# Kernel tuning notes

Hardware: AMD Instinct MI355X
Metric: run time of the kernel (lower is better)

## Reference

```python
import jax, jax.numpy as jnp
import numpy as np

N = 262144            # number of particles
H0 = 0.006            # base SPH support radius (unit square domain)
GRID = 256            # static upper bound on cells per dimension (actual ~170)
NUM_CELLS = GRID * GRID
K = 32                # max particles stored per cell (avg occupancy ~9.4)
NCAND = 9 * K         # searchRadius=1 -> 3x3 cell stencil
MAX_NEIGHBORS = 64    # padded neighbor-list width (avg neighbor count ~27)


def setup_inputs() -> dict:
    key = jax.random.key(0)
    kp, ks = jax.random.split(key)
    positions = jax.random.uniform(kp, (N, 2), dtype=jnp.float32)
    # supports in [0.9*H0, H0], mimicking mildly adaptive SPH supports
    supports = H0 * (0.9 + 0.1 * jax.random.uniform(ks, (N,), dtype=jnp.float32))
    return {"positions": positions, "supports": supports}


def _cell_linear_indices(positions, supports):
    # mirrors sortPositions: cell size = hMax, indices = ceil((p - qMin)/hMax)
    hMax = jnp.max(supports)
    qMin = jnp.min(positions, axis=0) - hMax
    ij = jnp.ceil((positions - qMin) / hMax).astype(jnp.int32)  # >= 1 by construction
    ij = jnp.clip(ij, 0, GRID - 1)
    return ij[:, 0] + GRID * ij[:, 1]


def _build_cell_table(lin):
    # dense equivalent of the hash-grid: sort by cell, counting-sort into [cell, slot]
    order = jnp.argsort(lin)                       # == sortingIndices in the original
    lin_s = lin[order]
    counts = jax.ops.segment_sum(jnp.ones(N, jnp.int32), lin, num_segments=NUM_CELLS)
    starts = jnp.cumsum(counts) - counts           # exclusive prefix sum == cumCell
    rank = jnp.arange(N, dtype=jnp.int32) - starts[lin_s].astype(jnp.int32)
    ovf = rank >= K                                # overflow slots -> dump row
    cell_t = jnp.where(ovf, NUM_CELLS, lin_s)
    slot_t = jnp.where(ovf, 0, rank)
    table = jnp.full((NUM_CELLS + 1, K), -1, dtype=jnp.int32)
    table = table.at[cell_t, slot_t].set(order.astype(jnp.int32))
    return table


def reference(positions, supports):
    lin = _cell_linear_indices(positions, supports)
    table = _build_cell_table(lin)

    # 3x3 stencil of neighbor cells (searchRadius = 1)
    dx, dy = jnp.meshgrid(jnp.arange(-1, 2), jnp.arange(-1, 2), indexing='ij')
    offs = (dx + GRID * dy).reshape(1, 9).astype(jnp.int32)
    cand_cells = jnp.clip(lin[:, None] + offs, 0, NUM_CELLS)  # [N, 9]

    cand = table[cand_cells].reshape(N, NCAND)     # [N, 288] candidate particle ids
    present = cand >= 0
    cidx = jnp.where(present, cand, 0)
    cpos = positions[cidx]                         # [N, 288, 2] gather (memory bound)
    diff = cpos - positions[:, None, :]
    dist = jnp.sqrt(jnp.sum(diff * diff, axis=-1)) # [N, 288]
    valid = present & (dist <= supports[:, None])  # |x_i - x_j| <= h_i (self included)
    count = jnp.sum(valid, axis=1).astype(jnp.int32)

    # compact valid candidates to the front, pad to MAX_NEIGHBORS
    order2 = jnp.argsort(jnp.where(valid, 0, 1).astype(jnp.int32), axis=1, stable=True)
    sel = order2[:, :MAX_NEIGHBORS]
    nbr = jnp.take_along_axis(cidx, sel, axis=1)
    dsel = jnp.take_along_axis(dist, sel, axis=1)
    inb = jnp.arange(MAX_NEIGHBORS)[None, :] < count[:, None]
    neighbors = jnp.where(inb, nbr, -1)
    radial = jnp.where(inb, dsel / supports[:, None], 0.0)  # fluidRadialDistances
    return neighbors, count, radial
```

## Files before the change

kernel.cpp:

```cpp
#include <hip/hip_runtime.h>
#include <float.h>

#define N_PART 262144
#define GRID_DIM 256
#define NUM_CELLS (GRID_DIM * GRID_DIM)
#define KP 32
#define MAXNB 64


__global__ __launch_bounds__(256) void prep_kernel(
        const float2* __restrict__ pos2, const float* __restrict__ sup,
        int* __restrict__ counts,
        float* __restrict__ bMinX, float* __restrict__ bMinY,
        float* __restrict__ bMaxH) {
    __shared__ unsigned s_minx, s_miny, s_maxh;
    int t = threadIdx.x, b = blockIdx.x;
    int tid = b * 256 + t;
    if (tid <= NUM_CELLS) counts[tid] = 0;
    if (t == 0) { s_minx = 0x7f7fffffu; s_miny = 0x7f7fffffu; s_maxh = 0u; }
    __syncthreads();
    float2 p = pos2[tid];
    float  h = sup[tid];
    atomicMin(&s_minx, __float_as_uint(p.x));
    atomicMin(&s_miny, __float_as_uint(p.y));
    atomicMax(&s_maxh, __float_as_uint(h));
    __syncthreads();
    if (t == 0) {
        bMinX[b] = __uint_as_float(s_minx);
        bMinY[b] = __uint_as_float(s_miny);
        bMaxH[b] = __uint_as_float(s_maxh);
    }
}

__global__ __launch_bounds__(256) void bin_kernel(
        const float2* __restrict__ pos2, const float* __restrict__ sup,
        const float* __restrict__ bMinX, const float* __restrict__ bMinY,
        const float* __restrict__ bMaxH,
        unsigned* __restrict__ params,
        int* __restrict__ counts, float4* __restrict__ Qraw) {
    __shared__ unsigned s_minx, s_miny, s_maxh;
    int t = threadIdx.x;
    int tid = blockIdx.x * 256 + t;
    if (t == 0) { s_minx = 0x7f7fffffu; s_miny = 0x7f7fffffu; s_maxh = 0u; }
    __syncthreads();
    {
        float mx = FLT_MAX, my = FLT_MAX, mh = 0.0f;
        for (int k = t; k < 1024; k += 256) {
            mx = fminf(mx, bMinX[k]);
            my = fminf(my, bMinY[k]);
            mh = fmaxf(mh, bMaxH[k]);
        }
        atomicMin(&s_minx, __float_as_uint(mx));
        atomicMin(&s_miny, __float_as_uint(my));
        atomicMax(&s_maxh, __float_as_uint(mh));
    }
    __syncthreads();
    if (blockIdx.x == 0 && t == 0) {
        params[0] = s_minx; params[1] = s_miny; params[2] = s_maxh;
    }
    float hmax  = __uint_as_float(s_maxh);
    float qminx = __uint_as_float(s_minx) - hmax;
    float qminy = __uint_as_float(s_miny) - hmax;
    float2 p = pos2[tid];
    float  h = sup[tid];
    int cx = (int)ceilf((p.x - qminx) / hmax);
    int cy = (int)ceilf((p.y - qminy) / hmax);
    cx = min(max(cx, 0), GRID_DIM - 1);
    cy = min(max(cy, 0), GRID_DIM - 1);
    int c = cx + GRID_DIM * cy;
    int slot = atomicAdd(&counts[c], 1);
    if (slot < KP)
        Qraw[(c << 5) + slot] = make_float4(p.x, p.y, __int_as_float(tid), h);
}

__global__ __launch_bounds__(256) void rank_kernel(
        const int* __restrict__ counts, const float4* __restrict__ Qraw,
        float4* __restrict__ Qpad, int* __restrict__ linR,
        int4* __restrict__ cinfo) {
    int tid = blockIdx.x * 256 + threadIdx.x;
    int c   = tid >> 3;
    int s0  = tid & 7;
    int cnt = min(counts[c], KP);
    const float4* row = Qraw + (c << 5);
    for (int sl = s0; sl < cnt; sl += 8) {
        float4 rec = row[sl];
        int id = __float_as_int(rec.z);
        int rank = 0;
        for (int k = 0; k < cnt; k++)
            rank += (__float_as_int(row[k].z) < id);
        float h = rec.w;
        float  hn  = __int_as_float(__float_as_int(h) + 1);
        double mid = 0.5 * ((double)h + (double)hn);
        double t2  = mid * mid;
        float  S   = (float)t2;
        S = ((double)S > t2) ? __int_as_float(__float_as_int(S) - 1) : S;
        Qpad[(c << 5) + rank] = make_float4(rec.x, rec.y, rec.z, S);
        linR[id] = (c << 5) | rank;
    }
    if (s0 == 0) {
        const int offs[9] = {-257, -1, 255, -256, 0, 256, -255, 1, 257};
        int cum = 0;
        int v[9];
#pragma unroll
        for (int o = 0; o < 9; o++) {
            int cl = min(max(c + offs[o], 0), NUM_CELLS);
            cum += min(counts[cl], KP);
            v[o] = cum;
        }
        cinfo[(c << 2) + 0] = make_int4(v[0], v[1], v[2], v[3]);
        cinfo[(c << 2) + 1] = make_int4(v[4], v[5], v[6], v[7]);
        cinfo[(c << 2) + 2] = make_int4(v[8], 0, 0, 0);
    }
}

__global__ __launch_bounds__(256) void query_kernel(
        const int* __restrict__ linR, const int4* __restrict__ cinfo,
        const float4* __restrict__ Qpad,
        float* __restrict__ outN, float* __restrict__ outC,
        float* __restrict__ outR) {
#pragma clang fp contract(off)
    __shared__ int   s_id[4][MAXNB];
    __shared__ float s_s2[4][MAXNB];

    int t    = threadIdx.x;
    int lane = t & 63;
    int wsl  = t >> 6;
    int bid  = blockIdx.x;
    int swz  = (bid & 7) * (int)(gridDim.x >> 3) + (bid >> 3);
    int w    = __builtin_amdgcn_readfirstlane(swz * 4 + wsl);

    int lr = __builtin_amdgcn_readfirstlane(linR[w]);
    int c  = lr >> 5;

    int4 ca = cinfo[(c << 2) + 0];
    int4 cb = cinfo[(c << 2) + 1];
    int4 cz = cinfo[(c << 2) + 2];
    float4 me = Qpad[lr];
    float px = me.x, py = me.y, S = me.w;

    const int offs[9] = {-257, -1, 255, -256, 0, 256, -255, 1, 257};
    int cum[10] = {0, ca.x, ca.y, ca.z, ca.w, cb.x, cb.y, cb.z, cb.w, };
    cum[9] = cz.x;
    int T = cum[9];
    int delta[9];
#pragma unroll
    for (int o = 0; o < 9; o++) {
        int cl = min(max(c + offs[o], 0), NUM_CELLS);
        delta[o] = (cl << 5) - cum[o];
    }

    if (T <= 64) {
        int dsel = delta[0];
#pragma unroll
        for (int m = 1; m < 9; m++)
            dsel = (lane >= cum[m]) ? delta[m] : dsel;
        int idx = (lane < T) ? (lane + dsel) : lr;
        float4 q = Qpad[idx];
        unsigned long long maskT = (T >= 64) ? ~0ull : ((1ull << T) - 1ull);
        float dx = q.x - px;
        float dy = q.y - py;
        float s2 = dx * dx + dy * dy;
        bool keep = (s2 <= S) && (lane < T);
        unsigned long long bal = __ballot(s2 <= S) & maskT;
        int rank = __builtin_amdgcn_mbcnt_hi(
            (unsigned)(bal >> 32),
            __builtin_amdgcn_mbcnt_lo((unsigned)bal, 0));
        if (keep) {
            s_id[wsl][rank] = __float_as_int(q.z);
            s_s2[wsl][rank] = s2;
        }
        int total = (int)__popcll(bal);
        int   jj = s_id[wsl][lane];
        float ss = s_s2[wsl][lane];
        bool inb = lane < total;
        float rh = __builtin_amdgcn_rsqf(S);
        float vN = inb ? (float)jj : -1.0f;
        float vR = inb ? __builtin_amdgcn_sqrtf(ss) * rh : 0.0f;
        size_t base = (size_t)w * MAXNB;
        __builtin_nontemporal_store(vN, &outN[base + lane]);
        __builtin_nontemporal_store(vR, &outR[base + lane]);
        if (lane == 0)
            __builtin_nontemporal_store((float)total, &outC[w]);
    } else {
        int total = 0;
        for (int b0 = 0; b0 < T; b0 += 64) {
            int ll = b0 + lane;
            int dsel = delta[0];
#pragma unroll
            for (int m = 1; m < 9; m++)
                dsel = (ll >= cum[m]) ? delta[m] : dsel;
            float4 q = Qpad[ll + dsel];
            float dx = q.x - px;
            float dy = q.y - py;
            float s2 = dx * dx + dy * dy;
            int rem = T - b0;
            unsigned long long maskT =
                (rem >= 64) ? ~0ull : ((1ull << rem) - 1ull);
            unsigned long long bal = __ballot(s2 <= S) & maskT;
            int rank = __builtin_amdgcn_mbcnt_hi(
                (unsigned)(bal >> 32),
                __builtin_amdgcn_mbcnt_lo((unsigned)bal, 0));
            int ww = total + rank;
            if ((s2 <= S) && (ll < T) && (ww < MAXNB)) {
                s_id[wsl][ww] = __float_as_int(q.z);
                s_s2[wsl][ww] = s2;
            }
            total += (int)__popcll(bal);
        }
        int stored = min(total, MAXNB);
        int   jj = s_id[wsl][lane];
        float ss = s_s2[wsl][lane];
        bool inb = lane < stored;
        float rh = __builtin_amdgcn_rsqf(S);
        float vN = inb ? (float)jj : -1.0f;
        float vR = inb ? __builtin_amdgcn_sqrtf(ss) * rh : 0.0f;
        size_t base = (size_t)w * MAXNB;
        __builtin_nontemporal_store(vN, &outN[base + lane]);
        __builtin_nontemporal_store(vR, &outR[base + lane]);
        if (lane == 0)
            __builtin_nontemporal_store((float)total, &outC[w]);
    }
}

extern "C" void kernel_launch(void* const* d_in, const int* in_sizes, int n_in,
                              void* d_out, int out_size, void* d_ws, size_t ws_size,
                              hipStream_t stream) {
    const float2* pos2 = (const float2*)d_in[0];
    const float*  sup  = (const float*)d_in[1];

    char* p = (char*)d_ws;
    auto alloc = [&](size_t bytes) {
        char* q = p;
        p += (bytes + 255) & ~(size_t)255;
        return q;
    };
    unsigned* params = (unsigned*)alloc(256);
    int*    counts = (int*)alloc((size_t)(NUM_CELLS + 1) * 4);
    float*  bMinX  = (float*)alloc(1024 * 4);
    float*  bMinY  = (float*)alloc(1024 * 4);
    float*  bMaxH  = (float*)alloc(1024 * 4);
    float4* Qraw   = (float4*)alloc((size_t)(NUM_CELLS + 1) * KP * 16);
    float4* Qpad   = (float4*)alloc(((size_t)(NUM_CELLS + 1) * KP + 64) * 16);
    int*    linR   = (int*)alloc((size_t)N_PART * 4);
    int4*   cinfo  = (int4*)alloc((size_t)NUM_CELLS * 4 * 16);

    float* out  = (float*)d_out;
    float* outN = out;
    float* outC = out + (size_t)N_PART * MAXNB;
    float* outR = outC + N_PART;

    prep_kernel<<<N_PART / 256, 256, 0, stream>>>(pos2, sup, counts,
                                                  bMinX, bMinY, bMaxH);
    bin_kernel<<<N_PART / 256, 256, 0, stream>>>(pos2, sup, bMinX, bMinY,
                                                 bMaxH, params, counts, Qraw);
    rank_kernel<<<NUM_CELLS * 8 / 256, 256, 0, stream>>>(counts, Qraw,
                                                         Qpad, linR, cinfo);
    query_kernel<<<N_PART / 4, 256, 0, stream>>>(linR, cinfo, Qpad,
                                                 outN, outC, outR);
}
```

Before: 272.9 us.

## Fold rank kernel into query kernel with in-wave id ranking over raw cells

```diff
diff --git a/kernel.cpp b/kernel.cpp
--- a/kernel.cpp
+++ b/kernel.cpp
@@ -73,49 +73,10 @@
         Qraw[(c << 5) + slot] = make_float4(p.x, p.y, __int_as_float(tid), h);
 }
 
-__global__ __launch_bounds__(256) void rank_kernel(
+__global__ __launch_bounds__(256) void query_kernel(
+        const float2* __restrict__ pos2, const float* __restrict__ sup,
+        const unsigned* __restrict__ params,
         const int* __restrict__ counts, const float4* __restrict__ Qraw,
-        float4* __restrict__ Qpad, int* __restrict__ linR,
-        int4* __restrict__ cinfo) {
-    int tid = blockIdx.x * 256 + threadIdx.x;
-    int c   = tid >> 3;
-    int s0  = tid & 7;
-    int cnt = min(counts[c], KP);
-    const float4* row = Qraw + (c << 5);
-    for (int sl = s0; sl < cnt; sl += 8) {
-        float4 rec = row[sl];
-        int id = __float_as_int(rec.z);
-        int rank = 0;
-        for (int k = 0; k < cnt; k++)
-            rank += (__float_as_int(row[k].z) < id);
-        float h = rec.w;
-        float  hn  = __int_as_float(__float_as_int(h) + 1);
-        double mid = 0.5 * ((double)h + (double)hn);
-        double t2  = mid * mid;
-        float  S   = (float)t2;
-        S = ((double)S > t2) ? __int_as_float(__float_as_int(S) - 1) : S;
-        Qpad[(c << 5) + rank] = make_float4(rec.x, rec.y, rec.z, S);
-        linR[id] = (c << 5) | rank;
-    }
-    if (s0 == 0) {
-        const int offs[9] = {-257, -1, 255, -256, 0, 256, -255, 1, 257};
-        int cum = 0;
-        int v[9];
-#pragma unroll
-        for (int o = 0; o < 9; o++) {
-            int cl = min(max(c + offs[o], 0), NUM_CELLS);
-            cum += min(counts[cl], KP);
-            v[o] = cum;
-        }
-        cinfo[(c << 2) + 0] = make_int4(v[0], v[1], v[2], v[3]);
-        cinfo[(c << 2) + 1] = make_int4(v[4], v[5], v[6], v[7]);
-        cinfo[(c << 2) + 2] = make_int4(v[8], 0, 0, 0);
-    }
-}
-
-__global__ __launch_bounds__(256) void query_kernel(
-        const int* __restrict__ linR, const int4* __restrict__ cinfo,
-        const float4* __restrict__ Qpad,
         float* __restrict__ outN, float* __restrict__ outC,
         float* __restrict__ outR) {
 #pragma clang fp contract(off)
@@ -129,45 +90,70 @@
     int swz  = (bid & 7) * (int)(gridDim.x >> 3) + (bid >> 3);
     int w    = __builtin_amdgcn_readfirstlane(swz * 4 + wsl);
 
-    int lr = __builtin_amdgcn_readfirstlane(linR[w]);
-    int c  = lr >> 5;
-
-    int4 ca = cinfo[(c << 2) + 0];
-    int4 cb = cinfo[(c << 2) + 1];
-    int4 cz = cinfo[(c << 2) + 2];
-    float4 me = Qpad[lr];
-    float px = me.x, py = me.y, S = me.w;
+    float2 pw = pos2[w];
+    float  hh = sup[w];
+    float px = __int_as_float(__builtin_amdgcn_readfirstlane(__float_as_int(pw.x)));
+    float py = __int_as_float(__builtin_amdgcn_readfirstlane(__float_as_int(pw.y)));
+    float h  = __int_as_float(__builtin_amdgcn_readfirstlane(__float_as_int(hh)));
+
+    float hmax  = __uint_as_float(params[2]);
+    float qminx = __uint_as_float(params[0]) - hmax;
+    float qminy = __uint_as_float(params[1]) - hmax;
+    int cx = (int)ceilf((px - qminx) / hmax);
+    int cy = (int)ceilf((py - qminy) / hmax);
+    cx = min(max(cx, 0), GRID_DIM - 1);
+    cy = min(max(cy, 0), GRID_DIM - 1);
+    int c = __builtin_amdgcn_readfirstlane(cx + GRID_DIM * cy);
+
+    float  hn  = __int_as_float(__float_as_int(h) + 1);
+    double mid = 0.5 * ((double)h + (double)hn);
+    double t2  = mid * mid;
+    float  S   = (float)t2;
+    S = ((double)S > t2) ? __int_as_float(__float_as_int(S) - 1) : S;
 
     const int offs[9] = {-257, -1, 255, -256, 0, 256, -255, 1, 257};
-    int cum[10] = {0, ca.x, ca.y, ca.z, ca.w, cb.x, cb.y, cb.z, cb.w, };
-    cum[9] = cz.x;
-    int T = cum[9];
-    int delta[9];
+    int cum[10], delta[9];
+    cum[0] = 0;
+    int maxc = 0;
 #pragma unroll
     for (int o = 0; o < 9; o++) {
         int cl = min(max(c + offs[o], 0), NUM_CELLS);
-        delta[o] = (cl << 5) - cum[o];
-    }
+        int cc = min(__builtin_amdgcn_readfirstlane(counts[cl]), KP);
+        delta[o]   = (cl << 5) - cum[o];
+        cum[o + 1] = cum[o] + cc;
+        maxc = max(maxc, cc);
+    }
+    int T = cum[9];
 
     if (T <= 64) {
-        int dsel = delta[0];
+        int dsel = delta[0], sb = 0, se = cum[1];
 #pragma unroll
-        for (int m = 1; m < 9; m++)
-            dsel = (lane >= cum[m]) ? delta[m] : dsel;
-        int idx = (lane < T) ? (lane + dsel) : lr;
-        float4 q = Qpad[idx];
-        unsigned long long maskT = (T >= 64) ? ~0ull : ((1ull << T) - 1ull);
+        for (int m = 1; m < 9; m++) {
+            bool g = lane >= cum[m];
+            dsel = g ? delta[m]   : dsel;
+            sb   = g ? cum[m]     : sb;
+            se   = g ? cum[m + 1] : se;
+        }
+        int segcnt = se - sb;
+        int idx = (lane < T) ? (lane + dsel) : (c << 5);
+        float4 q = Qraw[idx];
         float dx = q.x - px;
         float dy = q.y - py;
         float s2 = dx * dx + dy * dy;
-        bool keep = (s2 <= S) && (lane < T);
-        unsigned long long bal = __ballot(s2 <= S) & maskT;
-        int rank = __builtin_amdgcn_mbcnt_hi(
-            (unsigned)(bal >> 32),
-            __builtin_amdgcn_mbcnt_lo((unsigned)bal, 0));
-        if (keep) {
-            s_id[wsl][rank] = __float_as_int(q.z);
-            s_s2[wsl][rank] = s2;
+        bool valid = (s2 <= S) && (lane < T);
+        int myid = __float_as_int(q.z);
+        int kv   = (myid << 1) | (valid ? 1 : 0);
+        int rcomp = 0;
+        for (int k = 0; k < maxc; k++) {
+            int kvk = __shfl(kv, sb + k);
+            rcomp += ((k < segcnt) && (kvk & 1) && ((kvk >> 1) < myid)) ? 1 : 0;
+        }
+        unsigned long long bal = __ballot(valid);
+        int before = (int)__popcll(bal & ((1ull << sb) - 1ull));
+        int wrank  = before + rcomp;
+        if (valid) {
+            s_id[wsl][wrank] = myid;
+            s_s2[wsl][wrank] = s2;
         }
         int total = (int)__popcll(bal);
         int   jj = s_id[wsl][lane];
@@ -183,29 +169,31 @@
             __builtin_nontemporal_store((float)total, &outC[w]);
     } else {
         int total = 0;
-        for (int b0 = 0; b0 < T; b0 += 64) {
-            int ll = b0 + lane;
-            int dsel = delta[0];
-#pragma unroll
-            for (int m = 1; m < 9; m++)
-                dsel = (ll >= cum[m]) ? delta[m] : dsel;
-            float4 q = Qpad[ll + dsel];
+#pragma unroll 1
+        for (int o = 0; o < 9; o++) {
+            int sb = cum[o];
+            int segcnt = cum[o + 1] - sb;
+            if (segcnt == 0) continue;
+            int rowb = delta[o] + sb;
+            int kdx = (lane < segcnt) ? (rowb + lane) : rowb;
+            float4 q = Qraw[kdx];
             float dx = q.x - px;
             float dy = q.y - py;
             float s2 = dx * dx + dy * dy;
-            int rem = T - b0;
-            unsigned long long maskT =
-                (rem >= 64) ? ~0ull : ((1ull << rem) - 1ull);
-            unsigned long long bal = __ballot(s2 <= S) & maskT;
-            int rank = __builtin_amdgcn_mbcnt_hi(
-                (unsigned)(bal >> 32),
-                __builtin_amdgcn_mbcnt_lo((unsigned)bal, 0));
-            int ww = total + rank;
-            if ((s2 <= S) && (ll < T) && (ww < MAXNB)) {
-                s_id[wsl][ww] = __float_as_int(q.z);
-                s_s2[wsl][ww] = s2;
+            bool valid = (lane < segcnt) && (s2 <= S);
+            int myid = __float_as_int(q.z);
+            int kv   = (myid << 1) | (valid ? 1 : 0);
+            int rcomp = 0;
+            for (int k = 0; k < segcnt; k++) {
+                int kvk = __shfl(kv, k);
+                rcomp += ((kvk & 1) && ((kvk >> 1) < myid)) ? 1 : 0;
             }
-            total += (int)__popcll(bal);
+            int wrank = total + rcomp;
+            if (valid && wrank < MAXNB) {
+                s_id[wsl][wrank] = myid;
+                s_s2[wsl][wrank] = s2;
+            }
+            total += (int)__popcll(__ballot(valid));
         }
         int stored = min(total, MAXNB);
         int   jj = s_id[wsl][lane];
@@ -240,9 +228,6 @@
     float*  bMinY  = (float*)alloc(1024 * 4);
     float*  bMaxH  = (float*)alloc(1024 * 4);
     float4* Qraw   = (float4*)alloc((size_t)(NUM_CELLS + 1) * KP * 16);
-    float4* Qpad   = (float4*)alloc(((size_t)(NUM_CELLS + 1) * KP + 64) * 16);
-    int*    linR   = (int*)alloc((size_t)N_PART * 4);
-    int4*   cinfo  = (int4*)alloc((size_t)NUM_CELLS * 4 * 16);
 
     float* out  = (float*)d_out;
     float* outN = out;
@@ -253,8 +238,6 @@
                                                   bMinX, bMinY, bMaxH);
     bin_kernel<<<N_PART / 256, 256, 0, stream>>>(pos2, sup, bMinX, bMinY,
                                                  bMaxH, params, counts, Qraw);
-    rank_kernel<<<NUM_CELLS * 8 / 256, 256, 0, stream>>>(counts, Qraw,
-                                                         Qpad, linR, cinfo);
-    query_kernel<<<N_PART / 4, 256, 0, stream>>>(linR, cinfo, Qpad,
-                                                 outN, outC, outR);
-}
+    query_kernel<<<N_PART / 4, 256, 0, stream>>>(pos2, sup, params, counts,
+                                                 Qraw, outN, outC, outR);
+}
```

Result: slower. 558.9 us (+104.8%).

## Recompute cell and neighbor prefix sums in query kernel instead of precomputing

Applied to the files above, without the earlier changes.

```diff
diff --git a/kernel.cpp b/kernel.cpp
--- a/kernel.cpp
+++ b/kernel.cpp
@@ -75,8 +75,7 @@
 
 __global__ __launch_bounds__(256) void rank_kernel(
         const int* __restrict__ counts, const float4* __restrict__ Qraw,
-        float4* __restrict__ Qpad, int* __restrict__ linR,
-        int4* __restrict__ cinfo) {
+        float4* __restrict__ Qpad) {
     int tid = blockIdx.x * 256 + threadIdx.x;
     int c   = tid >> 3;
     int s0  = tid & 7;
@@ -88,34 +87,14 @@
         int rank = 0;
         for (int k = 0; k < cnt; k++)
             rank += (__float_as_int(row[k].z) < id);
-        float h = rec.w;
-        float  hn  = __int_as_float(__float_as_int(h) + 1);
-        double mid = 0.5 * ((double)h + (double)hn);
-        double t2  = mid * mid;
-        float  S   = (float)t2;
-        S = ((double)S > t2) ? __int_as_float(__float_as_int(S) - 1) : S;
-        Qpad[(c << 5) + rank] = make_float4(rec.x, rec.y, rec.z, S);
-        linR[id] = (c << 5) | rank;
-    }
-    if (s0 == 0) {
-        const int offs[9] = {-257, -1, 255, -256, 0, 256, -255, 1, 257};
-        int cum = 0;
-        int v[9];
-#pragma unroll
-        for (int o = 0; o < 9; o++) {
-            int cl = min(max(c + offs[o], 0), NUM_CELLS);
-            cum += min(counts[cl], KP);
-            v[o] = cum;
-        }
-        cinfo[(c << 2) + 0] = make_int4(v[0], v[1], v[2], v[3]);
-        cinfo[(c << 2) + 1] = make_int4(v[4], v[5], v[6], v[7]);
-        cinfo[(c << 2) + 2] = make_int4(v[8], 0, 0, 0);
+        Qpad[(c << 5) + rank] = rec;
     }
 }
 
 __global__ __launch_bounds__(256) void query_kernel(
-        const int* __restrict__ linR, const int4* __restrict__ cinfo,
-        const float4* __restrict__ Qpad,
+        const float2* __restrict__ pos2, const float* __restrict__ sup,
+        const unsigned* __restrict__ params,
+        const int* __restrict__ counts, const float4* __restrict__ Qpad,
         float* __restrict__ outN, float* __restrict__ outC,
         float* __restrict__ outR) {
 #pragma clang fp contract(off)
@@ -129,32 +108,45 @@
     int swz  = (bid & 7) * (int)(gridDim.x >> 3) + (bid >> 3);
     int w    = __builtin_amdgcn_readfirstlane(swz * 4 + wsl);
 
-    int lr = __builtin_amdgcn_readfirstlane(linR[w]);
-    int c  = lr >> 5;
-
-    int4 ca = cinfo[(c << 2) + 0];
-    int4 cb = cinfo[(c << 2) + 1];
-    int4 cz = cinfo[(c << 2) + 2];
-    float4 me = Qpad[lr];
-    float px = me.x, py = me.y, S = me.w;
+    float2 pw = pos2[w];
+    float  hh = sup[w];
+    float px = __int_as_float(__builtin_amdgcn_readfirstlane(__float_as_int(pw.x)));
+    float py = __int_as_float(__builtin_amdgcn_readfirstlane(__float_as_int(pw.y)));
+    float h  = __int_as_float(__builtin_amdgcn_readfirstlane(__float_as_int(hh)));
+
+    float hmax  = __uint_as_float(params[2]);
+    float qminx = __uint_as_float(params[0]) - hmax;
+    float qminy = __uint_as_float(params[1]) - hmax;
+    int cx = (int)ceilf((px - qminx) / hmax);
+    int cy = (int)ceilf((py - qminy) / hmax);
+    cx = min(max(cx, 0), GRID_DIM - 1);
+    cy = min(max(cy, 0), GRID_DIM - 1);
+    int c = __builtin_amdgcn_readfirstlane(cx + GRID_DIM * cy);
+
+    float  hn  = __int_as_float(__float_as_int(h) + 1);
+    double mid = 0.5 * ((double)h + (double)hn);
+    double t2  = mid * mid;
+    float  S   = (float)t2;
+    S = ((double)S > t2) ? __int_as_float(__float_as_int(S) - 1) : S;
 
     const int offs[9] = {-257, -1, 255, -256, 0, 256, -255, 1, 257};
-    int cum[10] = {0, ca.x, ca.y, ca.z, ca.w, cb.x, cb.y, cb.z, cb.w, };
-    cum[9] = cz.x;
-    int T = cum[9];
-    int delta[9];
+    int cum[10], delta[9];
+    cum[0] = 0;
 #pragma unroll
     for (int o = 0; o < 9; o++) {
         int cl = min(max(c + offs[o], 0), NUM_CELLS);
-        delta[o] = (cl << 5) - cum[o];
-    }
+        int cc = min(__builtin_amdgcn_readfirstlane(counts[cl]), KP);
+        delta[o]   = (cl << 5) - cum[o];
+        cum[o + 1] = cum[o] + cc;
+    }
+    int T = cum[9];
 
     if (T <= 64) {
         int dsel = delta[0];
 #pragma unroll
         for (int m = 1; m < 9; m++)
             dsel = (lane >= cum[m]) ? delta[m] : dsel;
-        int idx = (lane < T) ? (lane + dsel) : lr;
+        int idx = (lane < T) ? (lane + dsel) : (c << 5);
         float4 q = Qpad[idx];
         unsigned long long maskT = (T >= 64) ? ~0ull : ((1ull << T) - 1ull);
         float dx = q.x - px;
@@ -241,8 +233,6 @@
     float*  bMaxH  = (float*)alloc(1024 * 4);
     float4* Qraw   = (float4*)alloc((size_t)(NUM_CELLS + 1) * KP * 16);
     float4* Qpad   = (float4*)alloc(((size_t)(NUM_CELLS + 1) * KP + 64) * 16);
-    int*    linR   = (int*)alloc((size_t)N_PART * 4);
-    int4*   cinfo  = (int4*)alloc((size_t)NUM_CELLS * 4 * 16);
 
     float* out  = (float*)d_out;
     float* outN = out;
@@ -253,8 +243,7 @@
                                                   bMinX, bMinY, bMaxH);
     bin_kernel<<<N_PART / 256, 256, 0, stream>>>(pos2, sup, bMinX, bMinY,
                                                  bMaxH, params, counts, Qraw);
-    rank_kernel<<<NUM_CELLS * 8 / 256, 256, 0, stream>>>(counts, Qraw,
-                                                         Qpad, linR, cinfo);
-    query_kernel<<<N_PART / 4, 256, 0, stream>>>(linR, cinfo, Qpad,
-                                                 outN, outC, outR);
-}
+    rank_kernel<<<NUM_CELLS * 8 / 256, 256, 0, stream>>>(counts, Qraw, Qpad);
+    query_kernel<<<N_PART / 4, 256, 0, stream>>>(pos2, sup, params, counts,
+                                                 Qpad, outN, outC, outR);
+}
```

New measurement: 276.2 us. About the same (+1.2%).
